# Performance work log

Hardware: AMD Instinct MI355X
Metric: run time of the kernel (lower is better)

Reference implementation:

```python
import jax, jax.numpy as jnp
import numpy as np

NS, NT, NB, DIM, FEAT = 2048, 2048, 512, 256, 8


def elu(x):
    return jnp.where(x > 0, x, jnp.expm1(x))


def kernel_weights(x, base, Wf, bf, Ww, bw):
    # x: [N, DIM], base: [NB, DIM]; vectorized form of the per-row Kernel_P loop.
    f = x @ Wf.T + bf              # [N, FEAT]
    g = base @ Wf.T + bf           # [NB, FEAT]
    # w_s(cat[x_i, base_j]) = f_i . Ww[:FEAT] + g_j . Ww[FEAT:] + bw
    raw = (f @ Ww[0, :FEAT])[:, None] + (g @ Ww[0, FEAT:])[None, :] + bw[0]  # [N, NB]
    w = elu(raw)
    return w / jnp.mean(w, axis=1, keepdims=True)


def setup_inputs() -> dict:
    key = jax.random.key(0)
    ks = jax.random.split(key, 12)
    source_x = jax.random.normal(ks[0], (NS, DIM), jnp.float32)
    target_x = jax.random.normal(ks[1], (NT, DIM), jnp.float32)
    source_y = jax.random.normal(ks[2], (NS, 1), jnp.float32)
    target_y = jax.random.normal(ks[3], (NT, 1), jnp.float32)
    # joint PD Gram matrix so that cov (Schur complement) is PD for cholesky
    G = jax.random.normal(ks[4], (NS + NT, 1024), jnp.float32)
    J = G @ G.T / 1024.0 + jnp.eye(NS + NT, dtype=jnp.float32)
    k_ss = J[:NS, :NS]
    k_st = J[:NS, NS:]
    k_tt = J[NS:, NS:]
    # shared PD NNGP base kernel (k_s_base = k_t_base = k_st_base) -> joint kernel PSD
    H = jax.random.normal(ks[5], (NB, NB), jnp.float32)
    Kb = H @ H.T / NB + jnp.eye(NB, dtype=jnp.float32)
    base_s = jax.random.normal(ks[6], (NB, DIM), jnp.float32)
    base_t = jax.random.normal(ks[7], (NB, DIM), jnp.float32)
    sf = 1.0 / np.sqrt(DIM)
    Wf = jax.random.normal(ks[8], (FEAT, DIM), jnp.float32) * sf
    bf = jnp.zeros((FEAT,), jnp.float32)
    sw = 1.0 / np.sqrt(2 * FEAT)
    Ws = jax.random.normal(ks[9], (1, 2 * FEAT), jnp.float32) * sw
    bs = jnp.ones((1,), jnp.float32)   # bias=1 keeps elu weights well away from zero mean
    Wt = jax.random.normal(ks[10], (1, 2 * FEAT), jnp.float32) * sw
    bt = jnp.ones((1,), jnp.float32)
    noise_s_opt = jnp.ones((1,), jnp.float32)
    noise_t_opt = jnp.ones((1,), jnp.float32)
    return dict(source_x=source_x, source_y=source_y, target_x=target_x,
                target_y=target_y, k_ss=k_ss, k_tt=k_tt, k_st=k_st,
                noise_s_opt=noise_s_opt, noise_t_opt=noise_t_opt,
                Wf=Wf, bf=bf, Ws=Ws, bs=bs, Wt=Wt, bt=bt,
                Kb=Kb, base_s=base_s, base_t=base_t)


def reference(source_x, source_y, target_x, target_y, k_ss, k_tt, k_st,
              noise_s_opt, noise_t_opt, Wf, bf, Ws, bs, Wt, bt,
              Kb, base_s, base_t):
    noise_s = jnp.clip(noise_s_opt, 1e-05, 1.0)
    noise_t = jnp.clip(noise_t_opt, 1e-05, 1.0)
    ws = kernel_weights(source_x, base_s, Wf, bf, Ws, bs)   # [NS, NB]
    wt = kernel_weights(target_x, base_t, Wf, bf, Wt, bt)   # [NT, NB]
    wsK = ws @ Kb                                           # [NS, NB]
    K_src = k_ss * (wsK @ ws.T) + noise_s * jnp.eye(source_x.shape[0], dtype=source_x.dtype)
    K_tgt = k_tt * ((wt @ Kb) @ wt.T) + noise_t * jnp.eye(target_x.shape[0], dtype=target_x.dtype)
    K_cos = k_st * (wsK @ wt.T)                             # [NS, NT]
    K_src_inv = jnp.linalg.inv(K_src)
    mu = K_cos.T @ (K_src_inv @ source_y)                   # [NT, 1]
    cov = K_tgt - K_cos.T @ (K_src_inv @ K_cos)             # [NT, NT]
    L = jnp.linalg.cholesky(cov)
    r = target_y - mu
    quad = jnp.trace(r.T @ (jnp.linalg.inv(cov) @ r))
    loss = (0.5 * jnp.sum(jnp.log(jnp.diagonal(L)))
            + 0.5 * quad
            + 0.5 * source_x.shape[0] * np.log(2 * np.pi))
    return loss
```

## Files before the change

### kernel.cpp

```cpp
#include <hip/hip_runtime.h>
#include <hip/hip_bf16.h>
#include <math.h>

#define NS 2048
#define NB 512
#define DIMX 256
#define NFEAT 8
#define DPAD 129
#define BI 16
#define NBK 8
#define BST 40

typedef __attribute__((ext_vector_type(8))) short s16x8;
typedef __attribute__((ext_vector_type(4))) float f32x4;

__device__ __forceinline__ void split_bf16(float x, ushort& h, ushort& l) {
    uint u = __float_as_uint(x);
    h = (ushort)(u >> 16);
    float hf = __uint_as_float((uint)h << 16);
    float r = x - hf;
    l = (ushort)(__float_as_uint(r) >> 16);
}


__global__ __launch_bounds__(256) void prep_k(const float* __restrict__ Wf,
                                              const float* __restrict__ bf,
                                              const float* __restrict__ Ws,
                                              const float* __restrict__ Wt,
                                              float* __restrict__ wcomb,
                                              float* __restrict__ consts) {
    int d = threadIdx.x;
    float w0 = 0.f, w1 = 0.f, w2 = 0.f, w3 = 0.f;
#pragma unroll
    for (int k = 0; k < NFEAT; ++k) {
        float wf = Wf[k * DIMX + d];
        w0 += Ws[k] * wf;
        w1 += Ws[NFEAT + k] * wf;
        w2 += Wt[k] * wf;
        w3 += Wt[NFEAT + k] * wf;
    }
    wcomb[0 * DIMX + d] = w0;
    wcomb[1 * DIMX + d] = w1;
    wcomb[2 * DIMX + d] = w2;
    wcomb[3 * DIMX + d] = w3;
    if (d == 0) {
        float c0 = 0.f, c1 = 0.f, c2 = 0.f, c3 = 0.f;
#pragma unroll
        for (int k = 0; k < NFEAT; ++k) {
            c0 += Ws[k] * bf[k];
            c1 += Ws[NFEAT + k] * bf[k];
            c2 += Wt[k] * bf[k];
            c3 += Wt[NFEAT + k] * bf[k];
        }
        consts[0] = c0; consts[1] = c1; consts[2] = c2; consts[3] = c3;
    }
}

__global__ __launch_bounds__(256) void matvec_k(const float* __restrict__ X, int nrows,
                                                const float* __restrict__ wc,
                                                const float* __restrict__ consts, int cidx,
                                                float* __restrict__ out) {
    int wave = threadIdx.x >> 6, lane = threadIdx.x & 63;
    int row = blockIdx.x * 4 + wave;
    if (row >= nrows) return;
    const float* xr = X + (size_t)row * DIMX;
    float s = 0.f;
#pragma unroll
    for (int t = 0; t < 4; ++t) s += xr[lane + 64 * t] * wc[lane + 64 * t];
#pragma unroll
    for (int off = 32; off; off >>= 1) s += __shfl_down(s, off);
    if (lane == 0) out[row] = s + consts[cidx];
}

__global__ __launch_bounds__(256) void weights_k(const float* __restrict__ a,
                                                 const float* __restrict__ b,
                                                 const float* __restrict__ bw,
                                                 float* __restrict__ w) {
    __shared__ float red[256];
    int i = blockIdx.x, tid = threadIdx.x;
    float ai = a[i] + bw[0];
    float r1 = ai + b[tid];
    float r2 = ai + b[tid + 256];
    float e1 = r1 > 0.f ? r1 : expm1f(r1);
    float e2 = r2 > 0.f ? r2 : expm1f(r2);
    red[tid] = e1 + e2;
    __syncthreads();
    for (int s = 128; s; s >>= 1) {
        if (tid < s) red[tid] += red[tid + s];
        __syncthreads();
    }
    float scale = 512.f / red[0];
    w[(size_t)i * NB + tid] = e1 * scale;
    w[(size_t)i * NB + tid + 256] = e2 * scale;
}

__global__ __launch_bounds__(64) void init_flags_k(int* __restrict__ f) {
    f[threadIdx.x] = 0;
}

template <int TA, int TB>
__global__ __launch_bounds__(512) void gemm_bf_k(int M, int N, int K,
                                                 const float* __restrict__ A, int lda, size_t zoffA,
                                                 const float* __restrict__ B, int ldb, size_t zoffB,
                                                 float* __restrict__ C, int ldc, size_t zoffC,
                                                 const float* __restrict__ kmat, int ldk,
                                                 const float* __restrict__ noisep,
                                                 const float* __restrict__ kmat2,
                                                 const float* __restrict__ noisep2,
                                                 int mode, int row0, int col0, int flags) {
    __shared__ ushort Ah[128 * BST], Al[128 * BST], Bh[128 * BST], Bl[128 * BST];
    int bz = blockIdx.z;
    A += zoffA * bz; B += zoffB * bz; C += zoffC * bz;
    if (bz == 1) {
        if (kmat2) kmat = kmat2;
        if (noisep2) noisep = noisep2;
    }

    int gx = gridDim.x;
    int nwg = gx * gridDim.y;
    int flat = blockIdx.y * gx + blockIdx.x;
    int qq = nwg >> 3, rr = nwg & 7;
    int xcd = flat & 7, pos = flat >> 3;
    int swz = (xcd < rr) ? (xcd * (qq + 1) + pos)
                         : (rr * (qq + 1) + (xcd - rr) * qq + pos);
    int bm = swz / gx, bn = swz % gx;

    int rowBase = bm * 128, colBase = bn * 128;
    if ((flags & 1) && (rowBase + 127) < colBase) return;
    int Kend = (flags & 2) ? ((rowBase + 128 < K) ? rowBase + 128 : K) : K;
    int Kstart = (flags & 4) ? colBase : 0;

    int tid = threadIdx.x;
    int lane = tid & 63, wid = tid >> 6;
    int wr = wid >> 2, wc = wid & 3;
    int fr = lane & 15, fk = (lane >> 4) * 8;

    int sidx = tid >> 2;
    int sk0 = (tid & 3) * 8;

    float av[8], bv[8];
    auto loadAB = [&](int kk) {
        if (TA == 0) {
            const float* src = A + (size_t)(rowBase + sidx) * lda + kk + sk0;
            float4 v0 = *(const float4*)src;
            float4 v1 = *(const float4*)(src + 4);
            av[0] = v0.x; av[1] = v0.y; av[2] = v0.z; av[3] = v0.w;
            av[4] = v1.x; av[5] = v1.y; av[6] = v1.z; av[7] = v1.w;
        } else {
#pragma unroll
            for (int q = 0; q < 8; ++q)
                av[q] = A[(size_t)(kk + sk0 + q) * lda + rowBase + sidx];
        }
        if (TB == 0) {
#pragma unroll
            for (int q = 0; q < 8; ++q)
                bv[q] = B[(size_t)(kk + sk0 + q) * ldb + colBase + sidx];
        } else {
            const float* src = B + (size_t)(colBase + sidx) * ldb + kk + sk0;
            float4 v0 = *(const float4*)src;
            float4 v1 = *(const float4*)(src + 4);
            bv[0] = v0.x; bv[1] = v0.y; bv[2] = v0.z; bv[3] = v0.w;
            bv[4] = v1.x; bv[5] = v1.y; bv[6] = v1.z; bv[7] = v1.w;
        }
    };
    auto cvtStore = [&]() {
        uint hw[4], lw[4];
#pragma unroll
        for (int q = 0; q < 4; ++q) {
            ushort h0, l0, h1, l1;
            split_bf16(av[2 * q], h0, l0);
            split_bf16(av[2 * q + 1], h1, l1);
            hw[q] = (uint)h0 | ((uint)h1 << 16);
            lw[q] = (uint)l0 | ((uint)l1 << 16);
        }
        int idx = sidx * BST + sk0;
        *(uint4*)&Ah[idx] = make_uint4(hw[0], hw[1], hw[2], hw[3]);
        *(uint4*)&Al[idx] = make_uint4(lw[0], lw[1], lw[2], lw[3]);
#pragma unroll
        for (int q = 0; q < 4; ++q) {
            ushort h0, l0, h1, l1;
            split_bf16(bv[2 * q], h0, l0);
            split_bf16(bv[2 * q + 1], h1, l1);
            hw[q] = (uint)h0 | ((uint)h1 << 16);
            lw[q] = (uint)l0 | ((uint)l1 << 16);
        }
        *(uint4*)&Bh[idx] = make_uint4(hw[0], hw[1], hw[2], hw[3]);
        *(uint4*)&Bl[idx] = make_uint4(lw[0], lw[1], lw[2], lw[3]);
    };

    f32x4 acc[4][2];
#pragma unroll
    for (int m = 0; m < 4; ++m)
#pragma unroll
        for (int n = 0; n < 2; ++n) acc[m][n] = (f32x4){0.f, 0.f, 0.f, 0.f};

    int nt = (Kend - Kstart) >> 5;
    loadAB(Kstart);
    for (int t = 0; t < nt; ++t) {
        cvtStore();
        __syncthreads();
        if (t + 1 < nt) loadAB(Kstart + (t + 1) * 32);

        s16x8 ah[4], al[4], bh[2], bl[2];
#pragma unroll
        for (int m = 0; m < 4; ++m) {
            int off = (wr * 64 + m * 16 + fr) * BST + fk;
            ah[m] = *(const s16x8*)&Ah[off];
            al[m] = *(const s16x8*)&Al[off];
        }
#pragma unroll
        for (int n = 0; n < 2; ++n) {
            int off = (wc * 32 + n * 16 + fr) * BST + fk;
            bh[n] = *(const s16x8*)&Bh[off];
            bl[n] = *(const s16x8*)&Bl[off];
        }
#pragma unroll
        for (int m = 0; m < 4; ++m) {
#pragma unroll
            for (int n = 0; n < 2; ++n) {
                acc[m][n] = __builtin_amdgcn_mfma_f32_16x16x32_bf16(ah[m], bh[n], acc[m][n], 0, 0, 0);
                acc[m][n] = __builtin_amdgcn_mfma_f32_16x16x32_bf16(ah[m], bl[n], acc[m][n], 0, 0, 0);
                acc[m][n] = __builtin_amdgcn_mfma_f32_16x16x32_bf16(al[m], bh[n], acc[m][n], 0, 0, 0);
            }
        }
        __syncthreads();
    }

#pragma unroll
    for (int m = 0; m < 4; ++m) {
#pragma unroll
        for (int n = 0; n < 2; ++n) {
            int gj = colBase + wc * 32 + n * 16 + fr;
#pragma unroll
            for (int reg = 0; reg < 4; ++reg) {
                int gi = rowBase + wr * 64 + m * 16 + (lane >> 4) * 4 + reg;
                float v = acc[m][n][reg];
                if (mode == 1 || mode == 2) {
                    v *= kmat[(size_t)gi * ldk + gj];
                    if (mode == 1 && (row0 + gi) == (col0 + gj)) {
                        float ns = noisep[0];
                        ns = fminf(fmaxf(ns, 1e-5f), 1.0f);
                        v += ns;
                    }
                } else if (mode == 3) {
                    v = C[(size_t)gi * ldc + gj] - v;
                } else if (mode == 4) {
                    v = -v;
                }
                C[(size_t)gi * ldc + gj] = v;
            }
        }
    }
}

__global__ __launch_bounds__(512) void chol_step_k(float* __restrict__ A, int lda, int kb,
                                                   int* __restrict__ flag) {
    extern __shared__ float s[];
    __shared__ float Ps[2][16][132];
    __shared__ float pnl[128 * 17];
    __shared__ float xd[NBK][BI][BI + 1];
    __shared__ float wbuf[NBK - 1][BI][BI + 1];
    int tid = threadIdx.x;
    int lane = tid & 63, wid = tid >> 6;

    if (blockIdx.x == 0) {
        float* Ad = A + (size_t)kb * 128 * (lda + 1);
        for (int idx = tid; idx < 128 * 32; idx += 512) {
            int r = idx >> 5, c4 = (idx & 31) * 4;
            float4 v = *(const float4*)(Ad + (size_t)r * lda + c4);
            float* dst = s + (size_t)r * DPAD + c4;
            dst[0] = v.x; dst[1] = v.y; dst[2] = v.z; dst[3] = v.w;
        }
        __syncthreads();

        for (int pb = 0; pb < 8; ++pb) {
            int pc0 = pb * 16, pe = pc0 + 16, nr = 128 - pe;

            if (wid == 0) {
                int r = lane & 15;
                float a[16];
#pragma unroll
                for (int j = 0; j < 16; ++j) a[j] = s[(size_t)(pc0 + r) * DPAD + pc0 + j];
#pragma unroll
                for (int k = 0; k < 16; ++k) {
                    float dk = sqrtf(__shfl(a[k], k));
                    float inv = 1.0f / dk;
                    if (r == k) a[k] = dk;
                    else if (r > k) a[k] *= inv;
#pragma unroll
                    for (int j = k + 1; j < 16; ++j) {
                        float ljk = __shfl(a[k], j);
                        if (r >= j) a[j] -= a[k] * ljk;
                    }
                }
                if (lane < 16) {
#pragma unroll
                    for (int j = 0; j < 16; ++j)
                        s[(size_t)(pc0 + r) * DPAD + pc0 + j] = (j <= r) ? a[j] : 0.f;
                }
            }
            __syncthreads();

            if (nr > 0) {
                if (tid < nr) {
                    int i = pe + tid;
                    float* Lr = s + (size_t)i * DPAD + pc0;
                    float x[16];
#pragma unroll
                    for (int c = 0; c < 16; ++c) x[c] = Lr[c];
#pragma unroll
                    for (int c = 0; c < 16; ++c) {
                        float xc = x[c] / s[(size_t)(pc0 + c) * DPAD + pc0 + c];
                        x[c] = xc;
#pragma unroll
                        for (int t = c + 1; t < 16; ++t)
                            x[t] -= xc * s[(size_t)(pc0 + t) * DPAD + pc0 + c];
                    }
#pragma unroll
                    for (int c = 0; c < 16; ++c) {
                        Lr[c] = x[c];
                        pnl[i * 17 + c] = x[c];
                    }
                }
                __syncthreads();

                int njb = nr >> 2;
                int ntask = nr * njb;
                for (int task = tid; task < ntask; task += 512) {
                    int ti = task % nr;
                    int jb = task / nr;
                    int i = pe + ti;
                    int j0 = pe + jb * 4;
                    if (j0 <= i) {
                        float xi[16];
#pragma unroll
                        for (int t = 0; t < 16; ++t) xi[t] = pnl[i * 17 + t];
#pragma unroll
                        for (int jj = 0; jj < 4; ++jj) {
                            int j = j0 + jj;
                            if (j <= i) {
                                float acc = 0.f;
#pragma unroll
                                for (int t = 0; t < 16; ++t) acc += xi[t] * pnl[j * 17 + t];
                                s[(size_t)i * DPAD + j] -= acc;
                            }
                        }
                    }
                }
                __syncthreads();
            }
        }

        {
            int g = tid >> 4, l = tid & 15;
            if (g < NBK) {
                const float* Lb = s + (size_t)(g * BI) * DPAD + g * BI;
                for (int r = 0; r < BI; ++r) {
                    float acc = (r == l) ? 1.f : 0.f;
                    for (int t = l; t < r; ++t) acc -= Lb[r * DPAD + t] * xd[g][t][l];
                    xd[g][r][l] = (r >= l) ? acc / Lb[r * DPAD + r] : 0.f;
                }
            }
        }
        __syncthreads();

        for (int d = 1; d < NBK; ++d) {
            int npairs = NBK - d;
            for (int e = tid; e < npairs * 256; e += 512) {
                int p = e >> 8, ab = e & 255;
                int a2 = ab >> 4, b2 = ab & 15;
                int J = p, I = p + d;
                int Ibase = I * BI, Jbase = J * BI;
                float acc = 0.f;
                {
                    const float* Lr = s + (size_t)(Ibase + a2) * DPAD + Jbase;
                    for (int t = 0; t < BI; ++t) acc += Lr[t] * xd[J][t][b2];
                }
                for (int K = J + 1; K < I; ++K) {
                    int Kbase = K * BI;
                    const float* Lr = s + (size_t)(Ibase + a2) * DPAD + Kbase;
                    const float* Xc = s + (size_t)(Jbase + b2) * DPAD + Kbase;
                    for (int t = 0; t < BI; ++t) acc += Lr[t] * Xc[t];
                }
                wbuf[p][a2][b2] = acc;
            }
            __syncthreads();
            for (int e = tid; e < npairs * 256; e += 512) {
                int p = e >> 8, ab = e & 255;
                int a2 = ab >> 4, b2 = ab & 15;
                int J = p, I = p + d;
                float acc = 0.f;
                for (int t = 0; t < BI; ++t) acc += xd[I][a2][t] * wbuf[p][t][b2];
                s[(size_t)(J * BI + b2) * DPAD + I * BI + a2] = -acc;
            }
            __syncthreads();
        }

        for (int idx = tid; idx < 128 * 128; idx += 512) {
            int r = idx >> 7, c = idx & 127;
            float v;
            if (c > r) {
                v = 0.f;
            } else {
                int gr = r >> 4, gc = c >> 4;
                v = (gr == gc) ? xd[gr][r & 15][c & 15] : s[(size_t)c * DPAD + r];
            }
            Ad[(size_t)r * lda + c] = v;
        }
        __threadfence();
        __syncthreads();
        if (tid == 0) {
            __hip_atomic_store(flag, 1, __ATOMIC_RELEASE, __HIP_MEMORY_SCOPE_AGENT);
        }
        return;
    }

    if (tid == 0) {
        while (__hip_atomic_load(flag, __ATOMIC_ACQUIRE, __HIP_MEMORY_SCOPE_AGENT) == 0) {}
    }
    __syncthreads();
    __threadfence();

    float* Pb = A + (size_t)(kb + blockIdx.x) * 128 * lda + (size_t)kb * 128;
    const float* D = A + (size_t)kb * 128 * (lda + 1);

    for (int idx = tid; idx < 128 * 128; idx += 512) {
        int j = idx >> 7, k = idx & 127;
        s[(size_t)k * DPAD + j] = D[(size_t)j * lda + k];
    }

    int tx = tid & 31, ty = tid >> 5;
    float acc[8][4];
#pragma unroll
    for (int i = 0; i < 8; ++i)
#pragma unroll
        for (int j = 0; j < 4; ++j) acc[i][j] = 0.f;

    float rp[4];
    auto loadP = [&](int kk) {
        int row = tid >> 2, koff = (tid & 3) * 4;
        const float* src = Pb + (size_t)row * lda + kk + koff;
        float4 v = *(const float4*)src;
        rp[0] = v.x; rp[1] = v.y; rp[2] = v.z; rp[3] = v.w;
    };
    auto storeP = [&](int buf) {
        int row = tid >> 2, koff = (tid & 3) * 4;
#pragma unroll
        for (int q = 0; q < 4; ++q) Ps[buf][koff + q][row] = rp[q];
    };

    loadP(0);
    storeP(0);
    for (int t = 0; t < 8; ++t) {
        __syncthreads();
        int cur = t & 1;
        bool more = (t + 1 < 8);
        if (more) loadP((t + 1) * 16);
#pragma unroll
        for (int k = 0; k < 16; ++k) {
            float a[8], b[4];
            float4 t0 = *(const float4*)&Ps[cur][k][ty * 4];
            float4 t1 = *(const float4*)&Ps[cur][k][64 + ty * 4];
            float4 u0 = *(const float4*)&s[(size_t)(t * 16 + k) * DPAD + tx * 4];
            a[0] = t0.x; a[1] = t0.y; a[2] = t0.z; a[3] = t0.w;
            a[4] = t1.x; a[5] = t1.y; a[6] = t1.z; a[7] = t1.w;
            b[0] = u0.x; b[1] = u0.y; b[2] = u0.z; b[3] = u0.w;
#pragma unroll
            for (int i = 0; i < 8; ++i)
#pragma unroll
                for (int j = 0; j < 4; ++j) acc[i][j] += a[i] * b[j];
        }
        if (more) storeP(cur ^ 1);
    }
#pragma unroll
    for (int i = 0; i < 8; ++i) {
        int gi = ((i >> 2) << 6) + ty * 4 + (i & 3);
#pragma unroll
        for (int j = 0; j < 4; ++j) {
            Pb[(size_t)gi * lda + tx * 4 + j] = acc[i][j];
        }
    }
}

__global__ __launch_bounds__(256) void gemv_lower_k(const float* __restrict__ L, int ld,
                                                    const float* __restrict__ y,
                                                    float* __restrict__ z, int n) {
    int wave = threadIdx.x >> 6, lane = threadIdx.x & 63;
    int row = blockIdx.x * 4 + wave;
    if (row >= n) return;
    const float* Lr = L + (size_t)row * ld;
    float s = 0.f;
    for (int j = lane; j <= row; j += 64) s += Lr[j] * y[j];
#pragma unroll
    for (int off = 32; off; off >>= 1) s += __shfl_down(s, off);
    if (lane == 0) z[row] = s;
}

__global__ __launch_bounds__(256) void resid_part_k(const float* __restrict__ Z,
                                                    const float* __restrict__ zv,
                                                    float* __restrict__ part) {
    int j = blockIdx.x * 256 + threadIdx.x;
    int i0 = blockIdx.y * 64;
    float acc = 0.f;
    for (int i = i0; i < i0 + 64; ++i) acc += Z[(size_t)i * NS + j] * zv[i];
    part[(size_t)blockIdx.y * NS + j] = acc;
}

__global__ __launch_bounds__(256) void resid_fin_k(const float* __restrict__ part,
                                                   const float* __restrict__ ty,
                                                   float* __restrict__ r) {
    int j = blockIdx.x * 256 + threadIdx.x;
    float acc = 0.f;
    for (int q = 0; q < 32; ++q) acc += part[(size_t)q * NS + j];
    r[j] = ty[j] - acc;
}

__global__ __launch_bounds__(256) void loss_k(const float* __restrict__ Lc, int n, int ldl,
                                              float sign,
                                              const float* __restrict__ v,
                                              float* __restrict__ out) {
    __shared__ float red1[256];
    __shared__ float red2[256];
    int tid = threadIdx.x;
    float s1 = 0.f, s2 = 0.f;
    for (int i = tid; i < n; i += 256) {
        s1 += logf(Lc[(size_t)i * ldl + i]);
        float vi = v[i];
        s2 += vi * vi;
    }
    red1[tid] = s1;
    red2[tid] = s2;
    __syncthreads();
    for (int s = 128; s; s >>= 1) {
        if (tid < s) { red1[tid] += red1[tid + s]; red2[tid] += red2[tid + s]; }
        __syncthreads();
    }
    if (tid == 0) {
        out[0] = 0.5f * sign * red1[0] + 0.5f * red2[0] + 0.5f * (float)n * 1.8378770664093453f;
    }
}


static const size_t CHOL_LDS = (size_t)128 * DPAD * sizeof(float);

static void run_chol(float* A, int* flags, hipStream_t stream) {
    for (int kb = 0; kb < 16; ++kb) {
        int nrem = 15 - kb;
        chol_step_k<<<dim3(1 + nrem), 512, CHOL_LDS, stream>>>(A, NS, kb, flags + kb);
        if (nrem > 0) {
            float* P = A + (size_t)(kb + 1) * 128 * NS + kb * 128;
            float* Ct = A + (size_t)(kb + 1) * 128 * (NS + 1);
            gemm_bf_k<0, 1><<<dim3(nrem, nrem), 512, 0, stream>>>(
                nrem * 128, nrem * 128, 128, P, NS, 0, P, NS, 0, Ct, NS, 0,
                nullptr, 0, nullptr, nullptr, nullptr, 3, 0, 0, 1);
        }
    }
}

static void run_inv(float* A, float* T, hipStream_t stream) {
    for (int s = 128; s <= 1024; s <<= 1) {
        int np = NS / (2 * s);
        size_t zz = (size_t)2 * s * (NS + 1);
        size_t zt = (size_t)s * s;
        dim3 g(s / 128, s / 128, np);
        gemm_bf_k<0, 0><<<g, 512, 0, stream>>>(s, s, s, A + (size_t)s * NS, NS, zz,
                                               A, NS, zz, T, s, zt,
                                               nullptr, 0, nullptr, nullptr, nullptr,
                                               0, 0, 0, 4);
        gemm_bf_k<0, 0><<<g, 512, 0, stream>>>(s, s, s, A + (size_t)s * (NS + 1), NS, zz,
                                               T, s, zt, A + (size_t)s * NS, NS, zz,
                                               nullptr, 0, nullptr, nullptr, nullptr,
                                               4, 0, 0, 2);
    }
}

extern "C" void kernel_launch(void* const* d_in, const int* in_sizes, int n_in,
                              void* d_out, int out_size, void* d_ws, size_t ws_size,
                              hipStream_t stream) {
    const float* source_x = (const float*)d_in[0];
    const float* source_y = (const float*)d_in[1];
    const float* target_x = (const float*)d_in[2];
    const float* target_y = (const float*)d_in[3];
    const float* k_ss = (const float*)d_in[4];
    const float* k_tt = (const float*)d_in[5];
    const float* k_st = (const float*)d_in[6];
    const float* noise_s = (const float*)d_in[7];
    const float* noise_t = (const float*)d_in[8];
    const float* Wf = (const float*)d_in[9];
    const float* bf = (const float*)d_in[10];
    const float* Ws = (const float*)d_in[11];
    const float* bs = (const float*)d_in[12];
    const float* Wt = (const float*)d_in[13];
    const float* bt = (const float*)d_in[14];
    const float* Kb = (const float*)d_in[15];
    const float* base_s = (const float*)d_in[16];
    const float* base_t = (const float*)d_in[17];
    float* out = (float*)d_out;

    float* w = (float*)d_ws;
    const size_t M2 = (size_t)NS * NS;
    float* Ksrc = w;
    float* Kcos = w + M2;
    float* Ktgt = w + 2 * M2;
    float* stag = w + 3 * M2;
    float* wsb = stag;
    float* wtb = stag + (size_t)NS * NB;
    float* wsK = stag + 2 * (size_t)NS * NB;
    float* wtK = stag + 3 * (size_t)NS * NB;
    float* Z = stag;
    float* T = w + 4 * M2;
    float* sm = T + (size_t)1024 * 1024;
    float* wcomb = sm;
    float* consts = sm + 1024;
    float* a_s = sm + 1032;
    float* b_s = a_s + NS;
    float* a_t = b_s + NB;
    float* b_t = a_t + NS;
    float* rvec = b_t + NB;
    float* vvec = rvec + NS;
    float* z2 = vvec + NS;
    int* flags = (int*)(z2 + NS);

    init_flags_k<<<1, 64, 0, stream>>>(flags);

    prep_k<<<1, 256, 0, stream>>>(Wf, bf, Ws, Wt, wcomb, consts);
    matvec_k<<<NS / 4, 256, 0, stream>>>(source_x, NS, wcomb + 0 * DIMX, consts, 0, a_s);
    matvec_k<<<NB / 4, 256, 0, stream>>>(base_s, NB, wcomb + 1 * DIMX, consts, 1, b_s);
    matvec_k<<<NS / 4, 256, 0, stream>>>(target_x, NS, wcomb + 2 * DIMX, consts, 2, a_t);
    matvec_k<<<NB / 4, 256, 0, stream>>>(base_t, NB, wcomb + 3 * DIMX, consts, 3, b_t);
    weights_k<<<NS, 256, 0, stream>>>(a_s, b_s, bs, wsb);
    weights_k<<<NS, 256, 0, stream>>>(a_t, b_t, bt, wtb);

    gemm_bf_k<0, 0><<<dim3(NB / 128, NS / 128, 2), 512, 0, stream>>>(
        NS, NB, NB, wsb, NB, (size_t)NS * NB, Kb, NB, 0, wsK, NB, (size_t)NS * NB,
        nullptr, 0, nullptr, nullptr, nullptr, 0, 0, 0, 0);

    gemm_bf_k<0, 1><<<dim3(NS / 128, NS / 128, 2), 512, 0, stream>>>(
        NS, NS, NB, wsK, NB, (size_t)NS * NB, wsb, NB, (size_t)NS * NB, Ksrc, NS, 2 * M2,
        k_ss, NS, noise_s, k_tt, noise_t, 1, 0, 0, 0);
    gemm_bf_k<0, 1><<<dim3(NS / 128, NS / 128), 512, 0, stream>>>(
        NS, NS, NB, wsK, NB, 0, wtb, NB, 0, Kcos, NS, 0,
        k_st, NS, nullptr, nullptr, nullptr, 2, 0, 0, 0);

    run_chol(Ksrc, flags, stream);
    run_inv(Ksrc, T, stream);

    gemm_bf_k<0, 0><<<dim3(NS / 128, NS / 128), 512, 0, stream>>>(
        NS, NS, NS, Ksrc, NS, 0, Kcos, NS, 0, Z, NS, 0,
        nullptr, 0, nullptr, nullptr, nullptr, 0, 0, 0, 2);

    gemv_lower_k<<<NS / 4, 256, 0, stream>>>(Ksrc, NS, source_y, z2, NS);
    resid_part_k<<<dim3(NS / 256, 32), 256, 0, stream>>>(Z, z2, T);
    resid_fin_k<<<NS / 256, 256, 0, stream>>>(T, target_y, rvec);

    gemm_bf_k<1, 0><<<dim3(NS / 128, NS / 128), 512, 0, stream>>>(
        NS, NS, NS, Z, NS, 0, Z, NS, 0, Ktgt, NS, 0,
        nullptr, 0, nullptr, nullptr, nullptr, 3, 0, 0, 1);

    run_chol(Ktgt, flags + 16, stream);
    run_inv(Ktgt, T, stream);

    gemv_lower_k<<<NS / 4, 256, 0, stream>>>(Ktgt, NS, rvec, vvec, NS);
    loss_k<<<1, 256, 0, stream>>>(Ktgt, NS, NS, -1.0f, vvec, out);
}
```

Baseline: 4.802 ms.

## Fuse Cholesky trailing update into panel kernel with per-panel flag dependencies

The blocked Cholesky step used to launch a diagonal/panel kernel and then a separate trailing-matrix SYRK gemm. Both now run as one launch: extra blocks each take one lower-triangular trailing tile and spin on per-panel flags before doing a split-bf16 MFMA update in place. This removes one launch per step and lets trailing tiles start as soon as their two panels finish, not after the whole panel kernel. In exchange it relies on spin-waiting across blocks, which can deadlock if waiting blocks are resident before producer blocks. It also adds LDS usage to the panel kernel and needs a larger flags array.

```diff
diff --git a/kernel.cpp b/kernel.cpp
--- a/kernel.cpp
+++ b/kernel.cpp
@@ -94,7 +94,7 @@
     w[(size_t)i * NB + tid + 256] = e2 * scale;
 }
 
-__global__ __launch_bounds__(64) void init_flags_k(int* __restrict__ f) {
+__global__ __launch_bounds__(512) void init_flags_k(int* __restrict__ f) {
     f[threadIdx.x] = 0;
 }
 
@@ -253,13 +253,14 @@
     }
 }
 
-__global__ __launch_bounds__(512) void chol_step_k(float* __restrict__ A, int lda, int kb,
-                                                   int* __restrict__ flag) {
+__global__ __launch_bounds__(512) void chol_full_k(float* __restrict__ A, int lda, int kb,
+                                                   int nrem, int* __restrict__ flags) {
     extern __shared__ float s[];
     __shared__ float Ps[2][16][132];
     __shared__ float pnl[128 * 17];
     __shared__ float xd[NBK][BI][BI + 1];
     __shared__ float wbuf[NBK - 1][BI][BI + 1];
+    __shared__ ushort Ah[128 * BST], Al[128 * BST], Bh[128 * BST], Bl[128 * BST];
     int tid = threadIdx.x;
     int lane = tid & 63, wid = tid >> 6;
 
@@ -410,74 +411,193 @@
         __threadfence();
         __syncthreads();
         if (tid == 0) {
-            __hip_atomic_store(flag, 1, __ATOMIC_RELEASE, __HIP_MEMORY_SCOPE_AGENT);
+            __hip_atomic_store(flags, 1, __ATOMIC_RELEASE, __HIP_MEMORY_SCOPE_AGENT);
         }
         return;
     }
 
-    if (tid == 0) {
-        while (__hip_atomic_load(flag, __ATOMIC_ACQUIRE, __HIP_MEMORY_SCOPE_AGENT) == 0) {}
-    }
-    __syncthreads();
-    __threadfence();
-
-    float* Pb = A + (size_t)(kb + blockIdx.x) * 128 * lda + (size_t)kb * 128;
-    const float* D = A + (size_t)kb * 128 * (lda + 1);
-
-    for (int idx = tid; idx < 128 * 128; idx += 512) {
-        int j = idx >> 7, k = idx & 127;
-        s[(size_t)k * DPAD + j] = D[(size_t)j * lda + k];
-    }
-
-    int tx = tid & 31, ty = tid >> 5;
-    float acc[8][4];
-#pragma unroll
-    for (int i = 0; i < 8; ++i)
-#pragma unroll
-        for (int j = 0; j < 4; ++j) acc[i][j] = 0.f;
-
-    float rp[4];
-    auto loadP = [&](int kk) {
-        int row = tid >> 2, koff = (tid & 3) * 4;
-        const float* src = Pb + (size_t)row * lda + kk + koff;
-        float4 v = *(const float4*)src;
-        rp[0] = v.x; rp[1] = v.y; rp[2] = v.z; rp[3] = v.w;
-    };
-    auto storeP = [&](int buf) {
-        int row = tid >> 2, koff = (tid & 3) * 4;
-#pragma unroll
-        for (int q = 0; q < 4; ++q) Ps[buf][koff + q][row] = rp[q];
-    };
-
-    loadP(0);
-    storeP(0);
-    for (int t = 0; t < 8; ++t) {
-        __syncthreads();
-        int cur = t & 1;
-        bool more = (t + 1 < 8);
-        if (more) loadP((t + 1) * 16);
-#pragma unroll
-        for (int k = 0; k < 16; ++k) {
-            float a[8], b[4];
-            float4 t0 = *(const float4*)&Ps[cur][k][ty * 4];
-            float4 t1 = *(const float4*)&Ps[cur][k][64 + ty * 4];
-            float4 u0 = *(const float4*)&s[(size_t)(t * 16 + k) * DPAD + tx * 4];
-            a[0] = t0.x; a[1] = t0.y; a[2] = t0.z; a[3] = t0.w;
-            a[4] = t1.x; a[5] = t1.y; a[6] = t1.z; a[7] = t1.w;
-            b[0] = u0.x; b[1] = u0.y; b[2] = u0.z; b[3] = u0.w;
-#pragma unroll
-            for (int i = 0; i < 8; ++i)
-#pragma unroll
-                for (int j = 0; j < 4; ++j) acc[i][j] += a[i] * b[j];
-        }
-        if (more) storeP(cur ^ 1);
-    }
-#pragma unroll
-    for (int i = 0; i < 8; ++i) {
-        int gi = ((i >> 2) << 6) + ty * 4 + (i & 3);
-#pragma unroll
-        for (int j = 0; j < 4; ++j) {
-            Pb[(size_t)gi * lda + tx * 4 + j] = acc[i][j];
+    if ((int)blockIdx.x <= nrem) {
+        int p = blockIdx.x;
+        if (tid == 0) {
+            while (__hip_atomic_load(flags, __ATOMIC_ACQUIRE, __HIP_MEMORY_SCOPE_AGENT) == 0) {}
+        }
+        __syncthreads();
+        __threadfence();
+
+        float* Pb = A + (size_t)(kb + p) * 128 * lda + (size_t)kb * 128;
+        const float* D = A + (size_t)kb * 128 * (lda + 1);
+
+        for (int idx = tid; idx < 128 * 128; idx += 512) {
+            int j = idx >> 7, k = idx & 127;
+            s[(size_t)k * DPAD + j] = D[(size_t)j * lda + k];
+        }
+
+        int tx = tid & 31, ty = tid >> 5;
+        float acc[8][4];
+#pragma unroll
+        for (int i = 0; i < 8; ++i)
+#pragma unroll
+            for (int j = 0; j < 4; ++j) acc[i][j] = 0.f;
+
+        float rp[4];
+        auto loadP = [&](int kk) {
+            int row = tid >> 2, koff = (tid & 3) * 4;
+            const float* src = Pb + (size_t)row * lda + kk + koff;
+            float4 v = *(const float4*)src;
+            rp[0] = v.x; rp[1] = v.y; rp[2] = v.z; rp[3] = v.w;
+        };
+        auto storeP = [&](int buf) {
+            int row = tid >> 2, koff = (tid & 3) * 4;
+#pragma unroll
+            for (int q = 0; q < 4; ++q) Ps[buf][koff + q][row] = rp[q];
+        };
+
+        loadP(0);
+        storeP(0);
+        for (int t = 0; t < 8; ++t) {
+            __syncthreads();
+            int cur = t & 1;
+            bool more = (t + 1 < 8);
+            if (more) loadP((t + 1) * 16);
+#pragma unroll
+            for (int k = 0; k < 16; ++k) {
+                float a[8], b[4];
+                float4 t0 = *(const float4*)&Ps[cur][k][ty * 4];
+                float4 t1 = *(const float4*)&Ps[cur][k][64 + ty * 4];
+                float4 u0 = *(const float4*)&s[(size_t)(t * 16 + k) * DPAD + tx * 4];
+                a[0] = t0.x; a[1] = t0.y; a[2] = t0.z; a[3] = t0.w;
+                a[4] = t1.x; a[5] = t1.y; a[6] = t1.z; a[7] = t1.w;
+                b[0] = u0.x; b[1] = u0.y; b[2] = u0.z; b[3] = u0.w;
+#pragma unroll
+                for (int i = 0; i < 8; ++i)
+#pragma unroll
+                    for (int j = 0; j < 4; ++j) acc[i][j] += a[i] * b[j];
+            }
+            if (more) storeP(cur ^ 1);
+        }
+#pragma unroll
+        for (int i = 0; i < 8; ++i) {
+            int gi = ((i >> 2) << 6) + ty * 4 + (i & 3);
+#pragma unroll
+            for (int j = 0; j < 4; ++j) {
+                Pb[(size_t)gi * lda + tx * 4 + j] = acc[i][j];
+            }
+        }
+        __threadfence();
+        __syncthreads();
+        if (tid == 0) {
+            __hip_atomic_store(flags + p, 1, __ATOMIC_RELEASE, __HIP_MEMORY_SCOPE_AGENT);
+        }
+        return;
+    }
+
+    {
+        int t = blockIdx.x - 1 - nrem;
+        int jc = 0;
+        while (t >= nrem - jc) { t -= nrem - jc; ++jc; }
+        int i = 1 + jc + t, j = 1 + jc;
+
+        if (tid == 0) {
+            while (__hip_atomic_load(flags + i, __ATOMIC_ACQUIRE, __HIP_MEMORY_SCOPE_AGENT) == 0) {}
+            while (__hip_atomic_load(flags + j, __ATOMIC_ACQUIRE, __HIP_MEMORY_SCOPE_AGENT) == 0) {}
+        }
+        __syncthreads();
+        __threadfence();
+
+        const float* Pi = A + (size_t)(kb + i) * 128 * lda + (size_t)kb * 128;
+        const float* Pj = A + (size_t)(kb + j) * 128 * lda + (size_t)kb * 128;
+        float* Ct = A + (size_t)(kb + i) * 128 * lda + (size_t)(kb + j) * 128;
+
+        int wr = wid >> 2, wc = wid & 3;
+        int fr = lane & 15, fk = (lane >> 4) * 8;
+        int sidx = tid >> 2, sk0 = (tid & 3) * 8;
+
+        float av[8], bv[8];
+        auto loadAB = [&](int kk) {
+            const float* srcA = Pi + (size_t)sidx * lda + kk + sk0;
+            float4 v0 = *(const float4*)srcA;
+            float4 v1 = *(const float4*)(srcA + 4);
+            av[0] = v0.x; av[1] = v0.y; av[2] = v0.z; av[3] = v0.w;
+            av[4] = v1.x; av[5] = v1.y; av[6] = v1.z; av[7] = v1.w;
+            const float* srcB = Pj + (size_t)sidx * lda + kk + sk0;
+            float4 u0 = *(const float4*)srcB;
+            float4 u1 = *(const float4*)(srcB + 4);
+            bv[0] = u0.x; bv[1] = u0.y; bv[2] = u0.z; bv[3] = u0.w;
+            bv[4] = u1.x; bv[5] = u1.y; bv[6] = u1.z; bv[7] = u1.w;
+        };
+        auto cvtStore = [&]() {
+            uint hw[4], lw[4];
+#pragma unroll
+            for (int q = 0; q < 4; ++q) {
+                ushort h0, l0, h1, l1;
+                split_bf16(av[2 * q], h0, l0);
+                split_bf16(av[2 * q + 1], h1, l1);
+                hw[q] = (uint)h0 | ((uint)h1 << 16);
+                lw[q] = (uint)l0 | ((uint)l1 << 16);
+            }
+            int idx = sidx * BST + sk0;
+            *(uint4*)&Ah[idx] = make_uint4(hw[0], hw[1], hw[2], hw[3]);
+            *(uint4*)&Al[idx] = make_uint4(lw[0], lw[1], lw[2], lw[3]);
+#pragma unroll
+            for (int q = 0; q < 4; ++q) {
+                ushort h0, l0, h1, l1;
+                split_bf16(bv[2 * q], h0, l0);
+                split_bf16(bv[2 * q + 1], h1, l1);
+                hw[q] = (uint)h0 | ((uint)h1 << 16);
+                lw[q] = (uint)l0 | ((uint)l1 << 16);
+            }
+            *(uint4*)&Bh[idx] = make_uint4(hw[0], hw[1], hw[2], hw[3]);
+            *(uint4*)&Bl[idx] = make_uint4(lw[0], lw[1], lw[2], lw[3]);
+        };
+
+        f32x4 acc[4][2];
+#pragma unroll
+        for (int m = 0; m < 4; ++m)
+#pragma unroll
+            for (int n = 0; n < 2; ++n) acc[m][n] = (f32x4){0.f, 0.f, 0.f, 0.f};
+
+        loadAB(0);
+        for (int t5 = 0; t5 < 4; ++t5) {
+            cvtStore();
+            __syncthreads();
+            if (t5 + 1 < 4) loadAB((t5 + 1) * 32);
+
+            s16x8 ah[4], al[4], bh[2], bl[2];
+#pragma unroll
+            for (int m = 0; m < 4; ++m) {
+                int off = (wr * 64 + m * 16 + fr) * BST + fk;
+                ah[m] = *(const s16x8*)&Ah[off];
+                al[m] = *(const s16x8*)&Al[off];
+            }
+#pragma unroll
+            for (int n = 0; n < 2; ++n) {
+                int off = (wc * 32 + n * 16 + fr) * BST + fk;
+                bh[n] = *(const s16x8*)&Bh[off];
+                bl[n] = *(const s16x8*)&Bl[off];
+            }
+#pragma unroll
+            for (int m = 0; m < 4; ++m) {
+#pragma unroll
+                for (int n = 0; n < 2; ++n) {
+                    acc[m][n] = __builtin_amdgcn_mfma_f32_16x16x32_bf16(ah[m], bh[n], acc[m][n], 0, 0, 0);
+                    acc[m][n] = __builtin_amdgcn_mfma_f32_16x16x32_bf16(ah[m], bl[n], acc[m][n], 0, 0, 0);
+                    acc[m][n] = __builtin_amdgcn_mfma_f32_16x16x32_bf16(al[m], bh[n], acc[m][n], 0, 0, 0);
+                }
+            }
+            __syncthreads();
+        }
+
+#pragma unroll
+        for (int m = 0; m < 4; ++m) {
+#pragma unroll
+            for (int n = 0; n < 2; ++n) {
+                int gj = wc * 32 + n * 16 + fr;
+#pragma unroll
+                for (int reg = 0; reg < 4; ++reg) {
+                    int gi = wr * 64 + m * 16 + (lane >> 4) * 4 + reg;
+                    Ct[(size_t)gi * lda + gj] -= acc[m][n][reg];
+                }
+            }
         }
     }
 }
@@ -546,14 +666,9 @@
 static void run_chol(float* A, int* flags, hipStream_t stream) {
     for (int kb = 0; kb < 16; ++kb) {
         int nrem = 15 - kb;
-        chol_step_k<<<dim3(1 + nrem), 512, CHOL_LDS, stream>>>(A, NS, kb, flags + kb);
-        if (nrem > 0) {
-            float* P = A + (size_t)(kb + 1) * 128 * NS + kb * 128;
-            float* Ct = A + (size_t)(kb + 1) * 128 * (NS + 1);
-            gemm_bf_k<0, 1><<<dim3(nrem, nrem), 512, 0, stream>>>(
-                nrem * 128, nrem * 128, 128, P, NS, 0, P, NS, 0, Ct, NS, 0,
-                nullptr, 0, nullptr, nullptr, nullptr, 3, 0, 0, 1);
-        }
+        int ntrail = nrem * (nrem + 1) / 2;
+        chol_full_k<<<dim3(1 + nrem + ntrail), 512, CHOL_LDS, stream>>>(
+            A, NS, kb, nrem, flags + kb * 16);
     }
 }
 
@@ -621,7 +736,7 @@
     float* z2 = vvec + NS;
     int* flags = (int*)(z2 + NS);
 
-    init_flags_k<<<1, 64, 0, stream>>>(flags);
+    init_flags_k<<<1, 512, 0, stream>>>(flags);
 
     prep_k<<<1, 256, 0, stream>>>(Wf, bf, Ws, Wt, wcomb, consts);
     matvec_k<<<NS / 4, 256, 0, stream>>>(source_x, NS, wcomb + 0 * DIMX, consts, 0, a_s);
@@ -657,7 +772,7 @@
         NS, NS, NS, Z, NS, 0, Z, NS, 0, Ktgt, NS, 0,
         nullptr, 0, nullptr, nullptr, nullptr, 3, 0, 0, 1);
 
-    run_chol(Ktgt, flags + 16, stream);
+    run_chol(Ktgt, flags + 256, stream);
     run_inv(Ktgt, T, stream);
 
     gemv_lower_k<<<NS / 4, 256, 0, stream>>>(Ktgt, NS, rvec, vvec, NS);
```

Measured after the change: 6.163 ms. 1.28x slower.

## Replace target inverse and gemv with a dataflow blocked triangular solve

Applied to the files above, without the earlier changes.

Drops the full triangular inversion of the target Cholesky factor and the following lower-triangular gemv. A single dataflow kernel does the blocked work instead. Sixteen blocks handle the diagonal tiles, apparently already inverted by run_chol, and 120 blocks compute the off-diagonal partial products, linked by flag spin-waits. This removes an O(n^3) inversion on the target side in exchange for a serialized block chain, inter-block spin-waiting, and a deadlock risk if not all blocks are co-resident. The flag array grows to 512 entries.

```diff
diff --git a/kernel.cpp b/kernel.cpp
--- a/kernel.cpp
+++ b/kernel.cpp
@@ -94,7 +94,7 @@
     w[(size_t)i * NB + tid + 256] = e2 * scale;
 }
 
-__global__ __launch_bounds__(64) void init_flags_k(int* __restrict__ f) {
+__global__ __launch_bounds__(512) void init_flags_k(int* __restrict__ f) {
     f[threadIdx.x] = 0;
 }
 
@@ -482,6 +482,83 @@
     }
 }
 
+__global__ __launch_bounds__(256) void trsv_df_k(const float* __restrict__ A, int lda,
+                                                 const float* __restrict__ r,
+                                                 float* __restrict__ v,
+                                                 float* __restrict__ part,
+                                                 int* __restrict__ vflag,
+                                                 int* __restrict__ pflag) {
+    extern __shared__ float pls[];
+    __shared__ float vls[128];
+    __shared__ float red[256];
+    int tid = threadIdx.x;
+
+    if (blockIdx.x < 16) {
+        int kb = blockIdx.x;
+        int base = kb * 128;
+        const float* D = A + (size_t)base * lda + base;
+        for (int idx = tid; idx < 128 * 128; idx += 256)
+            pls[(size_t)(idx >> 7) * DPAD + (idx & 127)] = D[(size_t)(idx >> 7) * lda + (idx & 127)];
+        if (tid == 0) {
+            for (int c = 0; c < kb; ++c)
+                while (__hip_atomic_load(pflag + kb * 16 + c, __ATOMIC_ACQUIRE,
+                                         __HIP_MEMORY_SCOPE_AGENT) == 0)
+                    __builtin_amdgcn_s_sleep(1);
+        }
+        __syncthreads();
+        __threadfence();
+        if (tid < 128) {
+            float acc = r[base + tid];
+            for (int c = 0; c < kb; ++c) acc -= part[(size_t)(kb * 16 + c) * 128 + tid];
+            vls[tid] = acc;
+        }
+        __syncthreads();
+        int row = tid & 127, half = tid >> 7;
+        float acc = 0.f;
+        const float* pr = pls + (size_t)row * DPAD + half * 64;
+        const float* vv = vls + half * 64;
+#pragma unroll 8
+        for (int j = 0; j < 64; ++j) acc += pr[j] * vv[j];
+        red[tid] = acc;
+        __syncthreads();
+        if (tid < 128) v[base + tid] = red[tid] + red[tid + 128];
+        __syncthreads();
+        __threadfence();
+        if (tid == 0)
+            __hip_atomic_store(vflag + kb, 1, __ATOMIC_RELEASE, __HIP_MEMORY_SCOPE_AGENT);
+    } else {
+        int p0 = blockIdx.x - 16;
+        int kb = 1;
+        while (p0 >= kb) { p0 -= kb; ++kb; }
+        int c = p0;
+        const float* Lp = A + (size_t)kb * 128 * lda + (size_t)c * 128;
+        for (int idx = tid; idx < 128 * 128; idx += 256)
+            pls[(size_t)(idx >> 7) * DPAD + (idx & 127)] = Lp[(size_t)(idx >> 7) * lda + (idx & 127)];
+        if (tid == 0) {
+            while (__hip_atomic_load(vflag + c, __ATOMIC_ACQUIRE,
+                                     __HIP_MEMORY_SCOPE_AGENT) == 0)
+                __builtin_amdgcn_s_sleep(1);
+        }
+        __syncthreads();
+        __threadfence();
+        if (tid < 128) vls[tid] = v[c * 128 + tid];
+        __syncthreads();
+        int row = tid & 127, half = tid >> 7;
+        float acc = 0.f;
+        const float* pr = pls + (size_t)row * DPAD + half * 64;
+        const float* vv = vls + half * 64;
+#pragma unroll 8
+        for (int j = 0; j < 64; ++j) acc += pr[j] * vv[j];
+        red[tid] = acc;
+        __syncthreads();
+        if (tid < 128) part[(size_t)(kb * 16 + c) * 128 + tid] = red[tid] + red[tid + 128];
+        __syncthreads();
+        __threadfence();
+        if (tid == 0)
+            __hip_atomic_store(pflag + kb * 16 + c, 1, __ATOMIC_RELEASE, __HIP_MEMORY_SCOPE_AGENT);
+    }
+}
+
 __global__ __launch_bounds__(256) void gemv_lower_k(const float* __restrict__ L, int ld,
                                                     const float* __restrict__ y,
                                                     float* __restrict__ z, int n) {
@@ -621,7 +698,7 @@
     float* z2 = vvec + NS;
     int* flags = (int*)(z2 + NS);
 
-    init_flags_k<<<1, 64, 0, stream>>>(flags);
+    init_flags_k<<<1, 512, 0, stream>>>(flags);
 
     prep_k<<<1, 256, 0, stream>>>(Wf, bf, Ws, Wt, wcomb, consts);
     matvec_k<<<NS / 4, 256, 0, stream>>>(source_x, NS, wcomb + 0 * DIMX, consts, 0, a_s);
@@ -658,8 +735,8 @@
         nullptr, 0, nullptr, nullptr, nullptr, 3, 0, 0, 1);
 
     run_chol(Ktgt, flags + 16, stream);
-    run_inv(Ktgt, T, stream);
-
-    gemv_lower_k<<<NS / 4, 256, 0, stream>>>(Ktgt, NS, rvec, vvec, NS);
+
+    trsv_df_k<<<dim3(136), 256, CHOL_LDS, stream>>>(Ktgt, NS, rvec, vvec, T,
+                                                    flags + 32, flags + 48);
     loss_k<<<1, 256, 0, stream>>>(Ktgt, NS, NS, -1.0f, vvec, out);
 }
```

After: 4.907 ms. 2.2% more time.
